# Kernel tuning notes

Measured on AMD Instinct MI355X. Metric: run time of the kernel, lower is better.

## Reference

```python
import jax, jax.numpy as jnp
import numpy as np

B, C, G = 2, 256, 32
SPATIAL = (16, 16, 16)
EPS = 1e-5


def setup_inputs() -> dict:
    key = jax.random.key(0)
    ks = jax.random.split(key, 11)
    s = 1.0 / np.sqrt(C)
    x = jax.random.normal(ks[0], (B, C) + SPATIAL, dtype=jnp.float32)
    mk = lambda k: jax.random.normal(k, (C, C), dtype=jnp.float32) * s
    return {
        "x": x,
        "Wq": mk(ks[1]), "bq": jnp.zeros((C,), jnp.float32),
        "Wk": mk(ks[2]), "bk": jnp.zeros((C,), jnp.float32),
        "Wv": mk(ks[3]), "bv": jnp.zeros((C,), jnp.float32),
        "Wo": mk(ks[4]), "bo": jnp.zeros((C,), jnp.float32),
        "gamma": jnp.ones((C,), jnp.float32),
        "beta": jnp.zeros((C,), jnp.float32),
    }


def reference(x, Wq, bq, Wk, bk, Wv, bv, Wo, bo, gamma, beta):
    b, c = x.shape[0], x.shape[1]
    xf = x.reshape(b, c, -1)  # [B, C, N]

    def proj1x1(inp, W, bias):
        return jnp.einsum('oc,bcn->bon', W, inp) + bias[None, :, None]

    q = proj1x1(xf, Wq, bq)
    k = proj1x1(xf, Wk, bk)
    v = proj1x1(xf, Wv, bv)

    # qk[b, n, m] = sum_c q[b, c, n] * k[b, c, m]   (no 1/sqrt(C) scale, as in source)
    scores = jnp.einsum('bcn,bcm->bnm', q, k)
    w = jax.nn.softmax(scores, axis=-1)
    # h[b, c, n] = sum_m v[b, c, m] * w[b, n, m]
    h = jnp.einsum('bcm,bnm->bcn', v, w)
    h = proj1x1(h, Wo, bo)

    y = xf + h  # residual

    # GroupNorm over (channels-in-group, spatial)
    yg = y.reshape(b, G, c // G, -1)
    mu = jnp.mean(yg, axis=(2, 3), keepdims=True)
    var = jnp.var(yg, axis=(2, 3), keepdims=True)
    yn = ((yg - mu) * jax.lax.rsqrt(var + EPS)).reshape(b, c, -1)
    yn = yn * gamma[None, :, None] + beta[None, :, None]

    out = yn * jax.nn.sigmoid(yn)  # SiLU
    return out.reshape(x.shape)
```

## Files before the change

kernel.cpp:

```cpp
#include <hip/hip_runtime.h>
#include <hip/hip_bf16.h>

typedef _Float16 f16;
typedef __attribute__((ext_vector_type(4))) _Float16 f16x4;
typedef __attribute__((ext_vector_type(8))) _Float16 f16x8;
typedef __attribute__((ext_vector_type(4))) float f32x4;

#define CD 256
#define ND 4096
#define GD 32
#define KVB 32

__device__ __forceinline__ void gl_lds16(const f16* g, f16* l) {
    __builtin_amdgcn_global_load_lds(
        (const __attribute__((address_space(1))) unsigned int*)g,
        (__attribute__((address_space(3))) unsigned int*)l,
        16, 0, 0);
}

__global__ __launch_bounds__(256)
void k_proj_qkv(const float* __restrict__ x,
                const float* __restrict__ Wq, const float* __restrict__ bq,
                const float* __restrict__ Wk, const float* __restrict__ bk,
                const float* __restrict__ Wv, const float* __restrict__ bv,
                f16* __restrict__ Qt, f16* __restrict__ Kt, f16* __restrict__ Vb)
{
    __shared__ f16 As[64][40];
    __shared__ f16 Bs[64][40];
    __shared__ f16 Ts[64][72];

    const int t  = threadIdx.x;
    const int n0 = blockIdx.x * 64;
    const int o0 = blockIdx.y * 64;
    const int p  = blockIdx.z % 3;
    const int bb = blockIdx.z / 3;

    const float* W    = (p == 0) ? Wq : (p == 1) ? Wk : Wv;
    const float* bias = (p == 0) ? bq : (p == 1) ? bk : bv;

    const int w  = t >> 6;
    const int l  = t & 63;
    const int lr = l & 15;
    const int lg = l >> 4;
    const int wo = (w >> 1) * 32;
    const int wn = (w & 1) * 32;

    const int sl = t & 63;
    const int k8 = (t >> 6) * 8;

    f32x4 acc[2][2] = {};

    for (int ck = 0; ck < CD; ck += 32) {
        __syncthreads();
        {
            const float* s = W + (size_t)(o0 + sl) * CD + ck + k8;
            f16x8 v;
#pragma unroll
            for (int u = 0; u < 8; ++u) v[u] = (f16)s[u];
            *(f16x8*)&As[sl][k8] = v;
        }
        {
            const float* s = x + ((size_t)bb * CD + ck + k8) * ND + n0 + sl;
            f16x8 v;
#pragma unroll
            for (int u = 0; u < 8; ++u) v[u] = (f16)s[(size_t)u * ND];
            *(f16x8*)&Bs[sl][k8] = v;
        }
        __syncthreads();
        f16x8 a0 = *(const f16x8*)&As[wo + lr][lg * 8];
        f16x8 a1 = *(const f16x8*)&As[wo + 16 + lr][lg * 8];
        f16x8 b0 = *(const f16x8*)&Bs[wn + lr][lg * 8];
        f16x8 b1 = *(const f16x8*)&Bs[wn + 16 + lr][lg * 8];
        acc[0][0] = __builtin_amdgcn_mfma_f32_16x16x32_f16(a0, b0, acc[0][0], 0, 0, 0);
        acc[0][1] = __builtin_amdgcn_mfma_f32_16x16x32_f16(a0, b1, acc[0][1], 0, 0, 0);
        acc[1][0] = __builtin_amdgcn_mfma_f32_16x16x32_f16(a1, b0, acc[1][0], 0, 0, 0);
        acc[1][1] = __builtin_amdgcn_mfma_f32_16x16x32_f16(a1, b1, acc[1][1], 0, 0, 0);
    }

    if (p < 2) {
        __syncthreads();
#pragma unroll
        for (int so = 0; so < 2; ++so)
#pragma unroll
            for (int r = 0; r < 4; ++r) {
                int orow  = wo + so * 16 + lg * 4 + r;
                float bv_ = bias[o0 + orow];
#pragma unroll
                for (int sn = 0; sn < 2; ++sn)
                    Ts[orow][wn + sn * 16 + lr] = (f16)(acc[so][sn][r] + bv_);
            }
        __syncthreads();
        f16* dst = (p == 0) ? Qt : Kt;
        int n  = t >> 2;
        int o8 = (t & 3) * 16;
        f16 tmp[16];
#pragma unroll
        for (int u = 0; u < 16; ++u) tmp[u] = Ts[o8 + u][n];
        f16* g = dst + ((size_t)bb * ND + n0 + n) * CD + o0 + o8;
        *(f16x8*)g       = *(f16x8*)&tmp[0];
        *(f16x8*)(g + 8) = *(f16x8*)&tmp[8];
    } else {
#pragma unroll
        for (int so = 0; so < 2; ++so)
#pragma unroll
            for (int r = 0; r < 4; ++r) {
                int orow  = wo + so * 16 + lg * 4 + r;
                float bv_ = bias[o0 + orow];
#pragma unroll
                for (int sn = 0; sn < 2; ++sn) {
                    int ncol = wn + sn * 16 + lr;
                    Vb[((size_t)bb * CD + o0 + orow) * ND + n0 + ncol] =
                        (f16)(acc[so][sn][r] + bv_);
                }
            }
    }
}

template<int KSN>
__global__ __launch_bounds__(256, 2)
void k_attn(const f16* __restrict__ Qt, const f16* __restrict__ Kt,
            const f16* __restrict__ Vb, f16* __restrict__ Op,
            float* __restrict__ ml)
{
    __shared__ f16 Ks[2][32 * 256];
    __shared__ f16 Vs[2][256 * 32];
    __shared__ f16 Pl[4][32][40];

    const int t  = threadIdx.x;
    const int w  = t >> 6;
    const int l  = t & 63;
    const int lr = l & 15;
    const int lg = l >> 4;
    const int ks = blockIdx.y;
    const int bb = blockIdx.z;
    const int q0 = blockIdx.x * 128 + w * 32;

    f16x8 qf[2][8];
#pragma unroll
    for (int qs = 0; qs < 2; ++qs)
#pragma unroll
        for (int kc = 0; kc < 8; ++kc)
            qf[qs][kc] = *(const f16x8*)(Qt + ((size_t)bb * ND + q0 + qs * 16 + lr) * CD + kc * 32 + lg * 8);

    f32x4 oacc[2][16] = {};
    float row_m[2] = { -3.0e38f, -3.0e38f };
    float row_l[2] = { 0.f, 0.f };

    const int kv0 = ks * (ND / KSN);
    const f16* ktb = Kt + (size_t)bb * ND * CD;
    const f16* vbb = Vb + (size_t)bb * CD * ND;

    int koff[4], voff[4];
#pragma unroll
    for (int j = 0; j < 4; ++j) {
        int v   = (w * 4 + j) * 64 + l;
        int row = v >> 5;
        int ch  = (v & 31) ^ (row & 7);
        koff[j] = row * CD + ch * 8;
        int c   = v >> 2;
        int u   = (v & 3) ^ ((c >> 1) & 3);
        voff[j] = c * ND + u * 8;
    }

    auto stage = [&](int m0, int bi) {
#pragma unroll
        for (int j = 0; j < 4; ++j)
            gl_lds16(ktb + (size_t)m0 * CD + koff[j], &Ks[bi][(w * 4 + j) * 512]);
#pragma unroll
        for (int j = 0; j < 4; ++j)
            gl_lds16(vbb + m0 + voff[j], &Vs[bi][(w * 4 + j) * 512]);
    };

    stage(kv0, 0);
    __syncthreads();

    const int NIT = (ND / KSN) / KVB;
    for (int it = 0; it < NIT; ++it) {
        const int bi = it & 1;
        if (it + 1 < NIT) stage(kv0 + (it + 1) * KVB, bi ^ 1);

        f32x4 s[2][2] = {};
        __builtin_amdgcn_s_setprio(1);
#pragma unroll
        for (int kc = 0; kc < 8; ++kc) {
            int chs = ((kc * 4 + lg) ^ (lr & 7)) * 8;
            f16x8 k0 = *(const f16x8*)&Ks[bi][(lr) * 256 + chs];
            f16x8 k1 = *(const f16x8*)&Ks[bi][(16 + lr) * 256 + chs];
            s[0][0] = __builtin_amdgcn_mfma_f32_16x16x32_f16(k0, qf[0][kc], s[0][0], 0, 0, 0);
            s[1][0] = __builtin_amdgcn_mfma_f32_16x16x32_f16(k1, qf[0][kc], s[1][0], 0, 0, 0);
            s[0][1] = __builtin_amdgcn_mfma_f32_16x16x32_f16(k0, qf[1][kc], s[0][1], 0, 0, 0);
            s[1][1] = __builtin_amdgcn_mfma_f32_16x16x32_f16(k1, qf[1][kc], s[1][1], 0, 0, 0);
        }
        __builtin_amdgcn_s_setprio(0);

#pragma unroll
        for (int qs = 0; qs < 2; ++qs) {
            float pm = fmaxf(
                fmaxf(fmaxf(s[0][qs][0], s[0][qs][1]), fmaxf(s[0][qs][2], s[0][qs][3])),
                fmaxf(fmaxf(s[1][qs][0], s[1][qs][1]), fmaxf(s[1][qs][2], s[1][qs][3])));
            pm = fmaxf(pm, __shfl_xor(pm, 16));
            pm = fmaxf(pm, __shfl_xor(pm, 32));
            float nm = fmaxf(row_m[qs], pm);
            float sc = __expf(row_m[qs] - nm);
            float p0 = __expf(s[0][qs][0] - nm);
            float p1 = __expf(s[0][qs][1] - nm);
            float p2 = __expf(s[0][qs][2] - nm);
            float p3 = __expf(s[0][qs][3] - nm);
            float p4 = __expf(s[1][qs][0] - nm);
            float p5 = __expf(s[1][qs][1] - nm);
            float p6 = __expf(s[1][qs][2] - nm);
            float p7 = __expf(s[1][qs][3] - nm);
            float ps = ((p0 + p1) + (p2 + p3)) + ((p4 + p5) + (p6 + p7));
            ps += __shfl_xor(ps, 16);
            ps += __shfl_xor(ps, 32);
            bool chg = nm > row_m[qs];
            row_l[qs] = row_l[qs] * sc + ps;
            row_m[qs] = nm;
            if (__any(chg)) {
#pragma unroll
                for (int ct = 0; ct < 16; ++ct) {
                    oacc[qs][ct][0] *= sc; oacc[qs][ct][1] *= sc;
                    oacc[qs][ct][2] *= sc; oacc[qs][ct][3] *= sc;
                }
            }
            f16x4 pk0 = { (f16)p0, (f16)p1, (f16)p2, (f16)p3 };
            f16x4 pk1 = { (f16)p4, (f16)p5, (f16)p6, (f16)p7 };
            *(f16x4*)&Pl[w][qs * 16 + lr][lg * 4]      = pk0;
            *(f16x4*)&Pl[w][qs * 16 + lr][16 + lg * 4] = pk1;
        }

        f16x8 pf0 = *(const f16x8*)&Pl[w][lr][lg * 8];
        f16x8 pf1 = *(const f16x8*)&Pl[w][16 + lr][lg * 8];
        __builtin_amdgcn_s_setprio(1);
#pragma unroll
        for (int ct = 0; ct < 16; ++ct) {
            f16x8 vf = *(const f16x8*)&Vs[bi][(ct * 16 + lr) * 32 + ((lg ^ ((lr >> 1) & 3))) * 8];
            oacc[0][ct] = __builtin_amdgcn_mfma_f32_16x16x32_f16(vf, pf0, oacc[0][ct], 0, 0, 0);
            oacc[1][ct] = __builtin_amdgcn_mfma_f32_16x16x32_f16(vf, pf1, oacc[1][ct], 0, 0, 0);
        }
        __builtin_amdgcn_s_setprio(0);
        __syncthreads();
    }

#pragma unroll
    for (int qs = 0; qs < 2; ++qs)
#pragma unroll
        for (int ct = 0; ct < 16; ++ct)
#pragma unroll
            for (int r = 0; r < 4; ++r) {
                int cch = ct * 16 + lg * 4 + r;
                Op[(((size_t)ks * 2 + bb) * CD + cch) * ND + q0 + qs * 16 + lr] =
                    (f16)oacc[qs][ct][r];
            }
    if (lg == 0) {
#pragma unroll
        for (int qs = 0; qs < 2; ++qs) {
            int n = q0 + qs * 16 + lr;
            ml[((ks * 2 + bb) * 2 + 0) * ND + n] = row_m[qs];
            ml[((ks * 2 + bb) * 2 + 1) * ND + n] = row_l[qs];
        }
    }
}

template<int KSN>
__global__ __launch_bounds__(256)
void k_ml(const float* __restrict__ ml, float* __restrict__ wq)
{
    int i = blockIdx.x * 256 + threadIdx.x;
    int b = i / ND, n = i % ND;
    float m[KSN], lv[KSN];
#pragma unroll
    for (int ks = 0; ks < KSN; ++ks) {
        m[ks]  = ml[((ks * 2 + b) * 2 + 0) * ND + n];
        lv[ks] = ml[((ks * 2 + b) * 2 + 1) * ND + n];
    }
    float M = m[0];
#pragma unroll
    for (int ks = 1; ks < KSN; ++ks) M = fmaxf(M, m[ks]);
    float wgt[KSN], L = 0.f;
#pragma unroll
    for (int ks = 0; ks < KSN; ++ks) { wgt[ks] = __expf(m[ks] - M); L += wgt[ks] * lv[ks]; }
    float inv = 1.0f / L;
#pragma unroll
    for (int ks = 0; ks < KSN; ++ks)
        wq[(ks * 2 + b) * ND + n] = wgt[ks] * inv;
}

template<int KSN>
__global__ __launch_bounds__(256)
void k_comb(const f16* __restrict__ Op, const float* __restrict__ wq,
            f16* __restrict__ Hb)
{
    size_t i = (size_t)blockIdx.x * 256 + threadIdx.x;
    int n0 = (int)(i % (ND / 8)) * 8;
    int c  = (int)((i / (ND / 8)) % CD);
    int b  = (int)(i / ((size_t)CD * (ND / 8)));

    float acc[8] = {};
#pragma unroll
    for (int ks = 0; ks < KSN; ++ks) {
        f16x8 o = *(const f16x8*)(Op + (((size_t)ks * 2 + b) * CD + c) * ND + n0);
        const float* wp = wq + (ks * 2 + b) * ND + n0;
        float4 w0 = *(const float4*)wp;
        float4 w1 = *(const float4*)(wp + 4);
        acc[0] += w0.x * (float)o[0]; acc[1] += w0.y * (float)o[1];
        acc[2] += w0.z * (float)o[2]; acc[3] += w0.w * (float)o[3];
        acc[4] += w1.x * (float)o[4]; acc[5] += w1.y * (float)o[5];
        acc[6] += w1.z * (float)o[6]; acc[7] += w1.w * (float)o[7];
    }
    f16x8 h;
#pragma unroll
    for (int u = 0; u < 8; ++u) h[u] = (f16)acc[u];
    *(f16x8*)(Hb + ((size_t)b * CD + c) * ND + n0) = h;
}

__global__ __launch_bounds__(256)
void k_proj_o(const f16* __restrict__ Hb, const float* __restrict__ Wo,
              const float* __restrict__ bo, const float* __restrict__ x,
              float* __restrict__ Y)
{
    __shared__ f16 As[64][40];
    __shared__ f16 Bs[64][40];

    const int t  = threadIdx.x;
    const int n0 = blockIdx.x * 64;
    const int o0 = blockIdx.y * 64;
    const int bb = blockIdx.z;

    const int w  = t >> 6;
    const int l  = t & 63;
    const int lr = l & 15;
    const int lg = l >> 4;
    const int wo = (w >> 1) * 32;
    const int wn = (w & 1) * 32;

    const int sl = t & 63;
    const int k8 = (t >> 6) * 8;

    f32x4 acc[2][2] = {};

    for (int ck = 0; ck < CD; ck += 32) {
        __syncthreads();
        {
            const float* s = Wo + (size_t)(o0 + sl) * CD + ck + k8;
            f16x8 v;
#pragma unroll
            for (int u = 0; u < 8; ++u) v[u] = (f16)s[u];
            *(f16x8*)&As[sl][k8] = v;
        }
        {
            const f16* s = Hb + ((size_t)bb * CD + ck + k8) * ND + n0 + sl;
            f16x8 v;
#pragma unroll
            for (int u = 0; u < 8; ++u) v[u] = s[(size_t)u * ND];
            *(f16x8*)&Bs[sl][k8] = v;
        }
        __syncthreads();
        f16x8 a0 = *(const f16x8*)&As[wo + lr][lg * 8];
        f16x8 a1 = *(const f16x8*)&As[wo + 16 + lr][lg * 8];
        f16x8 b0 = *(const f16x8*)&Bs[wn + lr][lg * 8];
        f16x8 b1 = *(const f16x8*)&Bs[wn + 16 + lr][lg * 8];
        acc[0][0] = __builtin_amdgcn_mfma_f32_16x16x32_f16(a0, b0, acc[0][0], 0, 0, 0);
        acc[0][1] = __builtin_amdgcn_mfma_f32_16x16x32_f16(a0, b1, acc[0][1], 0, 0, 0);
        acc[1][0] = __builtin_amdgcn_mfma_f32_16x16x32_f16(a1, b0, acc[1][0], 0, 0, 0);
        acc[1][1] = __builtin_amdgcn_mfma_f32_16x16x32_f16(a1, b1, acc[1][1], 0, 0, 0);
    }

#pragma unroll
    for (int so = 0; so < 2; ++so)
#pragma unroll
        for (int r = 0; r < 4; ++r) {
            int orow  = wo + so * 16 + lg * 4 + r;
            float bv_ = bo[o0 + orow];
#pragma unroll
            for (int sn = 0; sn < 2; ++sn) {
                int ncol   = wn + sn * 16 + lr;
                size_t idx = ((size_t)bb * CD + o0 + orow) * ND + n0 + ncol;
                Y[idx] = acc[so][sn][r] + bv_ + x[idx];
            }
        }
}

__global__ __launch_bounds__(256)
void k_stats(const float* __restrict__ Y, float* __restrict__ stats)
{
    const int g = blockIdx.x, b = blockIdx.y;
    const float* base = Y + ((size_t)b * CD + g * 8) * ND;
    float s = 0.f, s2 = 0.f;
    for (int i = threadIdx.x; i < (8 * ND) / 4; i += 256) {
        float4 v = ((const float4*)base)[i];
        s  += v.x + v.y + v.z + v.w;
        s2 += v.x * v.x + v.y * v.y + v.z * v.z + v.w * v.w;
    }
#pragma unroll
    for (int m = 1; m < 64; m <<= 1) {
        s  += __shfl_xor(s, m);
        s2 += __shfl_xor(s2, m);
    }
    __shared__ float red[8];
    if ((threadIdx.x & 63) == 0) {
        red[(threadIdx.x >> 6) * 2]     = s;
        red[(threadIdx.x >> 6) * 2 + 1] = s2;
    }
    __syncthreads();
    if (threadIdx.x == 0) {
        float S  = red[0] + red[2] + red[4] + red[6];
        float S2 = red[1] + red[3] + red[5] + red[7];
        float mean = S / 32768.f;
        float var  = S2 / 32768.f - mean * mean;
        stats[(b * GD + g) * 2]     = mean;
        stats[(b * GD + g) * 2 + 1] = rsqrtf(var + 1e-5f);
    }
}

__global__ __launch_bounds__(256)
void k_norm_silu(const float* __restrict__ Y, const float* __restrict__ stats,
                 const float* __restrict__ gamma, const float* __restrict__ beta,
                 float* __restrict__ out)
{
    size_t i4 = (size_t)blockIdx.x * 256 + threadIdx.x;
    int c = (int)((i4 / (ND / 4)) % CD);
    int b = (int)(i4 / ((size_t)CD * (ND / 4)));
    float mean = stats[(b * GD + c / 8) * 2];
    float rstd = stats[(b * GD + c / 8) * 2 + 1];
    float ga = gamma[c], be = beta[c];
    float4 v = ((const float4*)Y)[i4];
    float in[4] = { v.x, v.y, v.z, v.w };
    float ob[4];
#pragma unroll
    for (int u = 0; u < 4; ++u) {
        float yn = (in[u] - mean) * rstd * ga + be;
        float sg = 1.0f / (1.0f + __expf(-yn));
        ob[u] = yn * sg;
    }
    *(float4*)(out + i4 * 4) = *(float4*)ob;
}

extern "C" void kernel_launch(void* const* d_in, const int* in_sizes, int n_in,
                              void* d_out, int out_size, void* d_ws, size_t ws_size,
                              hipStream_t stream)
{
    const float* x     = (const float*)d_in[0];
    const float* Wq    = (const float*)d_in[1];
    const float* bq    = (const float*)d_in[2];
    const float* Wk    = (const float*)d_in[3];
    const float* bk    = (const float*)d_in[4];
    const float* Wv    = (const float*)d_in[5];
    const float* bv    = (const float*)d_in[6];
    const float* Wo    = (const float*)d_in[7];
    const float* bo    = (const float*)d_in[8];
    const float* gamma = (const float*)d_in[9];
    const float* beta  = (const float*)d_in[10];

    char* ws = (char*)d_ws;
    f16* Qt = (f16*)(ws);
    f16* Kt = (f16*)(ws + (4u << 20));
    f16* Vb = (f16*)(ws + (8u << 20));
    f16* Hb = (f16*)(ws + (12u << 20));
    f16* Op = (f16*)(ws + (16u << 20));
    float* Y = (float*)(ws + (16u << 20));

    const bool big = ws_size >= (50ull << 20);

    k_proj_qkv<<<dim3(64, 4, 6), 256, 0, stream>>>(x, Wq, bq, Wk, bk, Wv, bv, Qt, Kt, Vb);

    if (big) {
        constexpr int KSN = 8;
        float* ml    = (float*)(ws + (48u << 20));
        float* wq    = (float*)(ws + (48u << 20) + (768u << 10));
        float* stats = (float*)(ws + (49u << 20) + (512u << 10));
        k_attn<KSN><<<dim3(32, KSN, 2), 256, 0, stream>>>(Qt, Kt, Vb, Op, ml);
        k_ml<KSN><<<dim3((2 * ND) / 256), 256, 0, stream>>>(ml, wq);
        k_comb<KSN><<<dim3((2 * CD * ND / 8) / 256), 256, 0, stream>>>(Op, wq, Hb);
        k_proj_o<<<dim3(64, 4, 2), 256, 0, stream>>>(Hb, Wo, bo, x, Y);
        k_stats<<<dim3(32, 2), 256, 0, stream>>>(Y, stats);
        k_norm_silu<<<2048, 256, 0, stream>>>(Y, stats, gamma, beta, (float*)d_out);
    } else {
        constexpr int KSN = 4;
        float* ml    = (float*)(ws + (32u << 20));
        float* wq    = (float*)(ws + (32u << 20) + (512u << 10));
        float* stats = (float*)(ws + (33u << 20));
        k_attn<KSN><<<dim3(32, KSN, 2), 256, 0, stream>>>(Qt, Kt, Vb, Op, ml);
        k_ml<KSN><<<dim3((2 * ND) / 256), 256, 0, stream>>>(ml, wq);
        k_comb<KSN><<<dim3((2 * CD * ND / 8) / 256), 256, 0, stream>>>(Op, wq, Hb);
        k_proj_o<<<dim3(64, 4, 2), 256, 0, stream>>>(Hb, Wo, bo, x, Y);
        k_stats<<<dim3(32, 2), 256, 0, stream>>>(Y, stats);
        k_norm_silu<<<2048, 256, 0, stream>>>(Y, stats, gamma, beta, (float*)d_out);
    }
}
```

Measured before the change: 121.3 us.

## Fuse QKV projections per block, remap attention grid to XCDs, lazy rescale, fuse GN+SiLU

The QKV projection now computes all three projections in one block, so the x tile is loaded and converted once instead of three times. The attention grid is flattened and remapped so blocks sharing a batch and KV split land on the same XCD, which may improve L2 reuse. The online softmax only rescales when the running max grows by more than a threshold, reducing exp and rescale work but letting exponent growth up to e^5 go unnormalized. GroupNorm stats and normalize+SiLU are fused into one kernel, removing a launch but leaving only 64 blocks for the elementwise pass.

```diff
diff --git a/kernel.cpp b/kernel.cpp
--- a/kernel.cpp
+++ b/kernel.cpp
@@ -25,18 +25,17 @@
                 const float* __restrict__ Wv, const float* __restrict__ bv,
                 f16* __restrict__ Qt, f16* __restrict__ Kt, f16* __restrict__ Vb)
 {
-    __shared__ f16 As[64][40];
+    __shared__ f16 As[3][64][40];
     __shared__ f16 Bs[64][40];
     __shared__ f16 Ts[64][72];
 
     const int t  = threadIdx.x;
     const int n0 = blockIdx.x * 64;
     const int o0 = blockIdx.y * 64;
-    const int p  = blockIdx.z % 3;
-    const int bb = blockIdx.z / 3;
-
-    const float* W    = (p == 0) ? Wq : (p == 1) ? Wk : Wv;
-    const float* bias = (p == 0) ? bq : (p == 1) ? bk : bv;
+    const int bb = blockIdx.z;
+
+    const float* Ws[3] = { Wq, Wk, Wv };
+    const float* bs[3] = { bq, bk, bv };
 
     const int w  = t >> 6;
     const int l  = t & 63;
@@ -48,16 +47,17 @@
     const int sl = t & 63;
     const int k8 = (t >> 6) * 8;
 
-    f32x4 acc[2][2] = {};
+    f32x4 acc[3][2][2] = {};
 
     for (int ck = 0; ck < CD; ck += 32) {
         __syncthreads();
-        {
-            const float* s = W + (size_t)(o0 + sl) * CD + ck + k8;
+#pragma unroll
+        for (int p = 0; p < 3; ++p) {
+            const float* s = Ws[p] + (size_t)(o0 + sl) * CD + ck + k8;
             f16x8 v;
 #pragma unroll
             for (int u = 0; u < 8; ++u) v[u] = (f16)s[u];
-            *(f16x8*)&As[sl][k8] = v;
+            *(f16x8*)&As[p][sl][k8] = v;
         }
         {
             const float* s = x + ((size_t)bb * CD + ck + k8) * ND + n0 + sl;
@@ -67,27 +67,31 @@
             *(f16x8*)&Bs[sl][k8] = v;
         }
         __syncthreads();
-        f16x8 a0 = *(const f16x8*)&As[wo + lr][lg * 8];
-        f16x8 a1 = *(const f16x8*)&As[wo + 16 + lr][lg * 8];
         f16x8 b0 = *(const f16x8*)&Bs[wn + lr][lg * 8];
         f16x8 b1 = *(const f16x8*)&Bs[wn + 16 + lr][lg * 8];
-        acc[0][0] = __builtin_amdgcn_mfma_f32_16x16x32_f16(a0, b0, acc[0][0], 0, 0, 0);
-        acc[0][1] = __builtin_amdgcn_mfma_f32_16x16x32_f16(a0, b1, acc[0][1], 0, 0, 0);
-        acc[1][0] = __builtin_amdgcn_mfma_f32_16x16x32_f16(a1, b0, acc[1][0], 0, 0, 0);
-        acc[1][1] = __builtin_amdgcn_mfma_f32_16x16x32_f16(a1, b1, acc[1][1], 0, 0, 0);
-    }
-
-    if (p < 2) {
+#pragma unroll
+        for (int p = 0; p < 3; ++p) {
+            f16x8 a0 = *(const f16x8*)&As[p][wo + lr][lg * 8];
+            f16x8 a1 = *(const f16x8*)&As[p][wo + 16 + lr][lg * 8];
+            acc[p][0][0] = __builtin_amdgcn_mfma_f32_16x16x32_f16(a0, b0, acc[p][0][0], 0, 0, 0);
+            acc[p][0][1] = __builtin_amdgcn_mfma_f32_16x16x32_f16(a0, b1, acc[p][0][1], 0, 0, 0);
+            acc[p][1][0] = __builtin_amdgcn_mfma_f32_16x16x32_f16(a1, b0, acc[p][1][0], 0, 0, 0);
+            acc[p][1][1] = __builtin_amdgcn_mfma_f32_16x16x32_f16(a1, b1, acc[p][1][1], 0, 0, 0);
+        }
+    }
+
+#pragma unroll
+    for (int p = 0; p < 2; ++p) {
         __syncthreads();
 #pragma unroll
         for (int so = 0; so < 2; ++so)
 #pragma unroll
             for (int r = 0; r < 4; ++r) {
                 int orow  = wo + so * 16 + lg * 4 + r;
-                float bv_ = bias[o0 + orow];
+                float bv_ = bs[p][o0 + orow];
 #pragma unroll
                 for (int sn = 0; sn < 2; ++sn)
-                    Ts[orow][wn + sn * 16 + lr] = (f16)(acc[so][sn][r] + bv_);
+                    Ts[orow][wn + sn * 16 + lr] = (f16)(acc[p][so][sn][r] + bv_);
             }
         __syncthreads();
         f16* dst = (p == 0) ? Qt : Kt;
@@ -99,21 +103,20 @@
         f16* g = dst + ((size_t)bb * ND + n0 + n) * CD + o0 + o8;
         *(f16x8*)g       = *(f16x8*)&tmp[0];
         *(f16x8*)(g + 8) = *(f16x8*)&tmp[8];
-    } else {
-#pragma unroll
-        for (int so = 0; so < 2; ++so)
-#pragma unroll
-            for (int r = 0; r < 4; ++r) {
-                int orow  = wo + so * 16 + lg * 4 + r;
-                float bv_ = bias[o0 + orow];
-#pragma unroll
-                for (int sn = 0; sn < 2; ++sn) {
-                    int ncol = wn + sn * 16 + lr;
-                    Vb[((size_t)bb * CD + o0 + orow) * ND + n0 + ncol] =
-                        (f16)(acc[so][sn][r] + bv_);
-                }
+    }
+#pragma unroll
+    for (int so = 0; so < 2; ++so)
+#pragma unroll
+        for (int r = 0; r < 4; ++r) {
+            int orow  = wo + so * 16 + lg * 4 + r;
+            float bv_ = bv[o0 + orow];
+#pragma unroll
+            for (int sn = 0; sn < 2; ++sn) {
+                int ncol = wn + sn * 16 + lr;
+                Vb[((size_t)bb * CD + o0 + orow) * ND + n0 + ncol] =
+                    (f16)(acc[2][so][sn][r] + bv_);
             }
-    }
+        }
 }
 
 template<int KSN>
@@ -131,9 +134,20 @@
     const int l  = t & 63;
     const int lr = l & 15;
     const int lg = l >> 4;
-    const int ks = blockIdx.y;
-    const int bb = blockIdx.z;
-    const int q0 = blockIdx.x * 128 + w * 32;
+
+    const int bid = blockIdx.x;
+    int bb, ks, qi;
+    if constexpr (KSN == 8) {
+        int xcd = bid & 7;
+        bb = xcd & 1;
+        ks = (xcd >> 1) | ((bid >> 8) << 2);
+        qi = (bid >> 3) & 31;
+    } else {
+        bb = bid & 1;
+        ks = (bid >> 1) & 3;
+        qi = bid >> 3;
+    }
+    const int q0 = qi * 128 + w * 32;
 
     f16x8 qf[2][8];
 #pragma unroll
@@ -200,8 +214,8 @@
                 fmaxf(fmaxf(s[1][qs][0], s[1][qs][1]), fmaxf(s[1][qs][2], s[1][qs][3])));
             pm = fmaxf(pm, __shfl_xor(pm, 16));
             pm = fmaxf(pm, __shfl_xor(pm, 32));
-            float nm = fmaxf(row_m[qs], pm);
-            float sc = __expf(row_m[qs] - nm);
+            bool need = (pm > row_m[qs] + 5.0f);
+            float nm  = need ? pm : row_m[qs];
             float p0 = __expf(s[0][qs][0] - nm);
             float p1 = __expf(s[0][qs][1] - nm);
             float p2 = __expf(s[0][qs][2] - nm);
@@ -213,16 +227,18 @@
             float ps = ((p0 + p1) + (p2 + p3)) + ((p4 + p5) + (p6 + p7));
             ps += __shfl_xor(ps, 16);
             ps += __shfl_xor(ps, 32);
-            bool chg = nm > row_m[qs];
-            row_l[qs] = row_l[qs] * sc + ps;
-            row_m[qs] = nm;
-            if (__any(chg)) {
+            if (__any(need)) {
+                float sc = __expf(row_m[qs] - nm);
+                row_l[qs] = row_l[qs] * sc + ps;
 #pragma unroll
                 for (int ct = 0; ct < 16; ++ct) {
                     oacc[qs][ct][0] *= sc; oacc[qs][ct][1] *= sc;
                     oacc[qs][ct][2] *= sc; oacc[qs][ct][3] *= sc;
                 }
+            } else {
+                row_l[qs] += ps;
             }
+            row_m[qs] = nm;
             f16x4 pk0 = { (f16)p0, (f16)p1, (f16)p2, (f16)p3 };
             f16x4 pk1 = { (f16)p4, (f16)p5, (f16)p6, (f16)p7 };
             *(f16x4*)&Pl[w][qs * 16 + lr][lg * 4]      = pk0;
@@ -382,13 +398,16 @@
 }
 
 __global__ __launch_bounds__(256)
-void k_stats(const float* __restrict__ Y, float* __restrict__ stats)
+void k_gn_silu(const float* __restrict__ Y, const float* __restrict__ gamma,
+               const float* __restrict__ beta, float* __restrict__ out)
 {
     const int g = blockIdx.x, b = blockIdx.y;
-    const float* base = Y + ((size_t)b * CD + g * 8) * ND;
+    const size_t base = ((size_t)b * CD + g * 8) * ND;
+    const float4* src = (const float4*)(Y + base);
+
     float s = 0.f, s2 = 0.f;
     for (int i = threadIdx.x; i < (8 * ND) / 4; i += 256) {
-        float4 v = ((const float4*)base)[i];
+        float4 v = src[i];
         s  += v.x + v.y + v.z + v.w;
         s2 += v.x * v.x + v.y * v.y + v.z * v.z + v.w * v.w;
     }
@@ -398,6 +417,7 @@
         s2 += __shfl_xor(s2, m);
     }
     __shared__ float red[8];
+    __shared__ float mr[2];
     if ((threadIdx.x & 63) == 0) {
         red[(threadIdx.x >> 6) * 2]     = s;
         red[(threadIdx.x >> 6) * 2 + 1] = s2;
@@ -408,32 +428,27 @@
         float S2 = red[1] + red[3] + red[5] + red[7];
         float mean = S / 32768.f;
         float var  = S2 / 32768.f - mean * mean;
-        stats[(b * GD + g) * 2]     = mean;
-        stats[(b * GD + g) * 2 + 1] = rsqrtf(var + 1e-5f);
-    }
-}
-
-__global__ __launch_bounds__(256)
-void k_norm_silu(const float* __restrict__ Y, const float* __restrict__ stats,
-                 const float* __restrict__ gamma, const float* __restrict__ beta,
-                 float* __restrict__ out)
-{
-    size_t i4 = (size_t)blockIdx.x * 256 + threadIdx.x;
-    int c = (int)((i4 / (ND / 4)) % CD);
-    int b = (int)(i4 / ((size_t)CD * (ND / 4)));
-    float mean = stats[(b * GD + c / 8) * 2];
-    float rstd = stats[(b * GD + c / 8) * 2 + 1];
-    float ga = gamma[c], be = beta[c];
-    float4 v = ((const float4*)Y)[i4];
-    float in[4] = { v.x, v.y, v.z, v.w };
-    float ob[4];
-#pragma unroll
-    for (int u = 0; u < 4; ++u) {
-        float yn = (in[u] - mean) * rstd * ga + be;
-        float sg = 1.0f / (1.0f + __expf(-yn));
-        ob[u] = yn * sg;
-    }
-    *(float4*)(out + i4 * 4) = *(float4*)ob;
+        mr[0] = mean;
+        mr[1] = rsqrtf(var + 1e-5f);
+    }
+    __syncthreads();
+    const float mean = mr[0], rstd = mr[1];
+
+    float4* dst = (float4*)(out + base);
+    for (int i = threadIdx.x; i < (8 * ND) / 4; i += 256) {
+        int c = g * 8 + (i >> 10);
+        float ga = gamma[c], be = beta[c];
+        float4 v = src[i];
+        float in[4] = { v.x, v.y, v.z, v.w };
+        float ob[4];
+#pragma unroll
+        for (int u = 0; u < 4; ++u) {
+            float yn = (in[u] - mean) * rstd * ga + be;
+            float sg = 1.0f / (1.0f + __expf(-yn));
+            ob[u] = yn * sg;
+        }
+        dst[i] = *(float4*)ob;
+    }
 }
 
 extern "C" void kernel_launch(void* const* d_in, const int* in_sizes, int n_in,
@@ -462,29 +477,25 @@
 
     const bool big = ws_size >= (50ull << 20);
 
-    k_proj_qkv<<<dim3(64, 4, 6), 256, 0, stream>>>(x, Wq, bq, Wk, bk, Wv, bv, Qt, Kt, Vb);
+    k_proj_qkv<<<dim3(64, 4, 2), 256, 0, stream>>>(x, Wq, bq, Wk, bk, Wv, bv, Qt, Kt, Vb);
 
     if (big) {
         constexpr int KSN = 8;
         float* ml    = (float*)(ws + (48u << 20));
         float* wq    = (float*)(ws + (48u << 20) + (768u << 10));
-        float* stats = (float*)(ws + (49u << 20) + (512u << 10));
-        k_attn<KSN><<<dim3(32, KSN, 2), 256, 0, stream>>>(Qt, Kt, Vb, Op, ml);
+        k_attn<KSN><<<dim3(32 * KSN * 2), 256, 0, stream>>>(Qt, Kt, Vb, Op, ml);
         k_ml<KSN><<<dim3((2 * ND) / 256), 256, 0, stream>>>(ml, wq);
         k_comb<KSN><<<dim3((2 * CD * ND / 8) / 256), 256, 0, stream>>>(Op, wq, Hb);
         k_proj_o<<<dim3(64, 4, 2), 256, 0, stream>>>(Hb, Wo, bo, x, Y);
-        k_stats<<<dim3(32, 2), 256, 0, stream>>>(Y, stats);
-        k_norm_silu<<<2048, 256, 0, stream>>>(Y, stats, gamma, beta, (float*)d_out);
+        k_gn_silu<<<dim3(GD, 2), 256, 0, stream>>>(Y, gamma, beta, (float*)d_out);
     } else {
         constexpr int KSN = 4;
         float* ml    = (float*)(ws + (32u << 20));
         float* wq    = (float*)(ws + (32u << 20) + (512u << 10));
-        float* stats = (float*)(ws + (33u << 20));
-        k_attn<KSN><<<dim3(32, KSN, 2), 256, 0, stream>>>(Qt, Kt, Vb, Op, ml);
+        k_attn<KSN><<<dim3(32 * KSN * 2), 256, 0, stream>>>(Qt, Kt, Vb, Op, ml);
         k_ml<KSN><<<dim3((2 * ND) / 256), 256, 0, stream>>>(ml, wq);
         k_comb<KSN><<<dim3((2 * CD * ND / 8) / 256), 256, 0, stream>>>(Op, wq, Hb);
         k_proj_o<<<dim3(64, 4, 2), 256, 0, stream>>>(Hb, Wo, bo, x, Y);
-        k_stats<<<dim3(32, 2), 256, 0, stream>>>(Y, stats);
-        k_norm_silu<<<2048, 256, 0, stream>>>(Y, stats, gamma, beta, (float*)d_out);
-    }
-}
+        k_gn_silu<<<dim3(GD, 2), 256, 0, stream>>>(Y, gamma, beta, (float*)d_out);
+    }
+}
```

Measured after the change: 121.2 us. Within noise of the previous version (-0.1%).
